# Optimization experiments

Measured on AMD Instinct MI355X. Metric: run time of the kernel, lower is better.

## Reference

```python
import jax, jax.numpy as jnp
import numpy as np

TOP_K = 2  # module default top_k


def setup_inputs() -> dict:
    key = jax.random.key(0)
    k1, k2, k3 = jax.random.split(key, 3)
    B, D, E = 4096, 1024, 64  # tokens, input_dim, num_experts
    return {
        "tensor1": jax.random.normal(k1, (B, D), dtype=jnp.float32),
        "tensor2": jax.random.normal(k2, (B, D), dtype=jnp.float32),
        "gate_weight": jax.random.normal(k3, (E, 2 * D), dtype=jnp.float32) * 0.02,
    }


def reference(tensor1, tensor2, gate_weight):
    # x: (B, 2D)
    x = jnp.concatenate((tensor1, tensor2), axis=-1)
    # pairwise L2 distance between each token and each expert vector
    diff = gate_weight[None, :, :] - x[:, None, :]          # (B, E, 2D)
    logits = -jnp.sqrt(jnp.sum(diff * diff, axis=-1))        # (B, E)
    topk_logits, indices = jax.lax.top_k(logits, TOP_K)      # (B, K)
    gating_weights = jax.nn.softmax(topk_logits, axis=-1)    # (B, K)
    rows = jnp.arange(logits.shape[0])[:, None]              # (B, 1)
    sparse_gating = jnp.zeros_like(logits).at[rows, indices].set(gating_weights)
    return sparse_gating
```

## Files before the change

### kernel.cpp

```cpp
#include <hip/hip_runtime.h>
#include <math.h>

#define NTOK 4096
#define NDIM 1024
#define KTOT 2048
#define NEXP 64
#define MT   64
#define KB   64
#define LSTR 72
#define NKC  16
#define NSTG 2

typedef _Float16 half8 __attribute__((ext_vector_type(8)));
typedef _Float16 half4 __attribute__((ext_vector_type(4)));
typedef float    floatx4 __attribute__((ext_vector_type(4)));

#define XSCALE 16.0f
#define WSCALE 1024.0f
#define INVSCALE (1.0f / (16.0f * 1024.0f))

struct h2pair { _Float16 h, l; };
__device__ __forceinline__ h2pair split2(float v) {
    h2pair r;
    r.h = (_Float16)v;
    r.l = (_Float16)(v - (float)r.h);
    return r;
}

__global__ __launch_bounds__(256, 4) void gemm_mfma(const float* __restrict__ t1,
                                                    const float* __restrict__ t2,
                                                    const float* __restrict__ W,
                                                    float* __restrict__ Gp,
                                                    float* __restrict__ Cp,
                                                    float* __restrict__ Wp) {
    __shared__ _Float16 Xh[MT * LSTR], Xl[MT * LSTR];
    __shared__ _Float16 Wh[NEXP * LSTR], Wl[NEXP * LSTR];

    const int tid  = threadIdx.x;
    const int lane = tid & 63;
    const int wv   = tid >> 6;
    const int srow = tid >> 4;
    const int scol = tid & 15;
    const int kc   = blockIdx.y;
    const int kbase = kc * (NSTG * KB);
    const int tok0  = blockIdx.x * MT;

    const float* __restrict__ xsrc = (kbase < NDIM)
        ? (t1 + (size_t)tok0 * NDIM + kbase)
        : (t2 + (size_t)tok0 * NDIM + (kbase - NDIM));
    const float* __restrict__ wsrc = W + kbase;

    floatx4 acc[4];
    #pragma unroll
    for (int j = 0; j < 4; ++j) { acc[j][0] = 0.f; acc[j][1] = 0.f; acc[j][2] = 0.f; acc[j][3] = 0.f; }
    float ssx[4] = {0.f, 0.f, 0.f, 0.f};
    float ssw[4] = {0.f, 0.f, 0.f, 0.f};

    const int frow = lane & 15;
    const int fq   = lane >> 4;
    const _Float16* xh_p = Xh + (16 * wv + frow) * LSTR + fq * 8;
    const _Float16* xl_p = Xl + (16 * wv + frow) * LSTR + fq * 8;

    #pragma unroll
    for (int s = 0; s < NSTG; ++s) {
        #pragma unroll
        for (int i = 0; i < 4; ++i) {
            const int row = srow + 16 * i;
            const float4 xv = *reinterpret_cast<const float4*>(
                xsrc + (size_t)row * NDIM + s * KB + scol * 4);
            const float4 wq = *reinterpret_cast<const float4*>(
                wsrc + (size_t)row * KTOT + s * KB + scol * 4);
            ssx[i] = fmaf(xv.x, xv.x, fmaf(xv.y, xv.y, fmaf(xv.z, xv.z, fmaf(xv.w, xv.w, ssx[i]))));
            ssw[i] = fmaf(wq.x, wq.x, fmaf(wq.y, wq.y, fmaf(wq.z, wq.z, fmaf(wq.w, wq.w, ssw[i]))));
            const h2pair x0 = split2(xv.x * XSCALE), x1 = split2(xv.y * XSCALE);
            const h2pair x2 = split2(xv.z * XSCALE), x3 = split2(xv.w * XSCALE);
            const h2pair w0 = split2(wq.x * WSCALE), w1 = split2(wq.y * WSCALE);
            const h2pair w2 = split2(wq.z * WSCALE), w3 = split2(wq.w * WSCALE);
            half4 hx, lx, hw, lw;
            hx[0] = x0.h; hx[1] = x1.h; hx[2] = x2.h; hx[3] = x3.h;
            lx[0] = x0.l; lx[1] = x1.l; lx[2] = x2.l; lx[3] = x3.l;
            hw[0] = w0.h; hw[1] = w1.h; hw[2] = w2.h; hw[3] = w3.h;
            lw[0] = w0.l; lw[1] = w1.l; lw[2] = w2.l; lw[3] = w3.l;
            *reinterpret_cast<half4*>(Xh + row * LSTR + scol * 4) = hx;
            *reinterpret_cast<half4*>(Xl + row * LSTR + scol * 4) = lx;
            *reinterpret_cast<half4*>(Wh + row * LSTR + scol * 4) = hw;
            *reinterpret_cast<half4*>(Wl + row * LSTR + scol * 4) = lw;
        }
        __syncthreads();

        #pragma unroll
        for (int ks = 0; ks < 2; ++ks) {
            const int ko = ks * 32;
            const half8 ah = *reinterpret_cast<const half8*>(xh_p + ko);
            const half8 al = *reinterpret_cast<const half8*>(xl_p + ko);
            half8 bh[4], bl[4];
            #pragma unroll
            for (int j = 0; j < 4; ++j) {
                bh[j] = *reinterpret_cast<const half8*>(Wh + (16 * j + frow) * LSTR + fq * 8 + ko);
                bl[j] = *reinterpret_cast<const half8*>(Wl + (16 * j + frow) * LSTR + fq * 8 + ko);
            }
            #pragma unroll
            for (int j = 0; j < 4; ++j)
                acc[j] = __builtin_amdgcn_mfma_f32_16x16x32_f16(ah, bh[j], acc[j], 0, 0, 0);
            #pragma unroll
            for (int j = 0; j < 4; ++j)
                acc[j] = __builtin_amdgcn_mfma_f32_16x16x32_f16(al, bh[j], acc[j], 0, 0, 0);
            #pragma unroll
            for (int j = 0; j < 4; ++j)
                acc[j] = __builtin_amdgcn_mfma_f32_16x16x32_f16(ah, bl[j], acc[j], 0, 0, 0);
        }
        __syncthreads();
    }

    const int m0 = 16 * wv + fq * 4;
    #pragma unroll
    for (int j = 0; j < 4; ++j) {
        #pragma unroll
        for (int i = 0; i < 4; ++i) {
            Gp[((size_t)kc * NTOK + tok0 + m0 + i) * NEXP + 16 * j + frow] = acc[j][i] * INVSCALE;
        }
    }

    #pragma unroll
    for (int off = 1; off < 16; off <<= 1) {
        #pragma unroll
        for (int i = 0; i < 4; ++i) {
            ssx[i] += __shfl_xor(ssx[i], off, 64);
            ssw[i] += __shfl_xor(ssw[i], off, 64);
        }
    }
    if (scol == 0) {
        #pragma unroll
        for (int i = 0; i < 4; ++i)
            Cp[(size_t)kc * NTOK + tok0 + srow + 16 * i] = ssx[i];
        if (blockIdx.x == 0) {
            #pragma unroll
            for (int i = 0; i < 4; ++i)
                Wp[kc * NEXP + srow + 16 * i] = ssw[i];
        }
    }
}

__global__ __launch_bounds__(256) void finalize(const float* __restrict__ Gp,
                                                const float* __restrict__ Cp,
                                                const float* __restrict__ Wp,
                                                float* __restrict__ out) {
    const int wv = threadIdx.x >> 6, lane = threadIdx.x & 63;
    const int token = blockIdx.x * 4 + wv;

    float gsum = 0.f, csum = 0.f, nv = 0.f;
    #pragma unroll
    for (int cix = 0; cix < NKC; ++cix) {
        gsum += Gp[((size_t)cix * NTOK + token) * NEXP + lane];
        csum += Cp[(size_t)cix * NTOK + token];
        nv   += Wp[cix * NEXP + lane];
    }

    const float S = fmaf(-2.f, gsum, csum) + nv;
    const float logit = -sqrtf(S);

    float v1 = logit; int i1 = lane;
    #pragma unroll
    for (int off = 32; off > 0; off >>= 1) {
        float ov = __shfl_xor(v1, off, 64);
        int   oi = __shfl_xor(i1, off, 64);
        if (ov > v1 || (ov == v1 && oi < i1)) { v1 = ov; i1 = oi; }
    }
    float v2 = (lane == i1) ? -__builtin_inff() : logit;
    int   i2 = lane;
    #pragma unroll
    for (int off = 32; off > 0; off >>= 1) {
        float ov = __shfl_xor(v2, off, 64);
        int   oi = __shfl_xor(i2, off, 64);
        if (ov > v2 || (ov == v2 && oi < i2)) { v2 = ov; i2 = oi; }
    }
    const float e2  = expf(v2 - v1);
    const float inv = 1.f / (1.f + e2);
    const float o = (lane == i1) ? inv : ((lane == i2) ? e2 * inv : 0.f);
    out[(size_t)token * NEXP + lane] = o;
}

extern "C" void kernel_launch(void* const* d_in, const int* in_sizes, int n_in,
                              void* d_out, int out_size, void* d_ws, size_t ws_size,
                              hipStream_t stream) {
    const float* t1 = (const float*)d_in[0];
    const float* t2 = (const float*)d_in[1];
    const float* W  = (const float*)d_in[2];
    float* out = (float*)d_out;

    float* Gp = (float*)d_ws;
    float* Cp = Gp + (size_t)NKC * NTOK * NEXP;
    float* Wp = Cp + (size_t)NKC * NTOK;

    gemm_mfma<<<dim3(NTOK / MT, NKC), 256, 0, stream>>>(t1, t2, W, Gp, Cp, Wp);
    finalize<<<NTOK / 4, 256, 0, stream>>>(Gp, Cp, Wp, out);
}
```

Baseline: 89.05 us.

## Precompute split fp16 gate weights once and halve K-split partials

Adds a prep kernel that converts the gate weights into hi/lo fp16 halves and computes the expert norms once, instead of every GEMM block reconverting the fp32 weights. The GEMM then loads the pre-split fp16 weights directly into shared memory. The K-split count drops from 16 to 8 with 4 stages per block, which halves the partial-sum traffic that finalize reads. The cost is an extra kernel launch, fewer blocks in the GEMM grid (512 instead of 1024), and launch bounds relaxed from 4 to 3.

```diff
diff --git a/kernel.cpp b/kernel.cpp
--- a/kernel.cpp
+++ b/kernel.cpp
@@ -8,8 +8,8 @@
 #define MT   64
 #define KB   64
 #define LSTR 72
-#define NKC  16
-#define NSTG 2
+#define NKC  8
+#define NSTG 4
 
 typedef _Float16 half8 __attribute__((ext_vector_type(8)));
 typedef _Float16 half4 __attribute__((ext_vector_type(4)));
@@ -27,12 +27,42 @@
     return r;
 }
 
-__global__ __launch_bounds__(256, 4) void gemm_mfma(const float* __restrict__ t1,
+__global__ __launch_bounds__(256) void prep_w(const float* __restrict__ W,
+                                              _Float16* __restrict__ Whg,
+                                              _Float16* __restrict__ Wlg,
+                                              float* __restrict__ nrm) {
+    const int e = blockIdx.x, t = threadIdx.x;
+    const float* row = W + (size_t)e * KTOT + t * 8;
+    const float4 a = *reinterpret_cast<const float4*>(row);
+    const float4 b = *reinterpret_cast<const float4*>(row + 4);
+    float ss = fmaf(a.x, a.x, fmaf(a.y, a.y, fmaf(a.z, a.z, fmaf(a.w, a.w, 0.f))));
+    ss = fmaf(b.x, b.x, fmaf(b.y, b.y, fmaf(b.z, b.z, fmaf(b.w, b.w, ss))));
+
+    const h2pair p0 = split2(a.x * WSCALE), p1 = split2(a.y * WSCALE);
+    const h2pair p2 = split2(a.z * WSCALE), p3 = split2(a.w * WSCALE);
+    const h2pair p4 = split2(b.x * WSCALE), p5 = split2(b.y * WSCALE);
+    const h2pair p6 = split2(b.z * WSCALE), p7 = split2(b.w * WSCALE);
+    half8 h, l;
+    h[0]=p0.h; h[1]=p1.h; h[2]=p2.h; h[3]=p3.h; h[4]=p4.h; h[5]=p5.h; h[6]=p6.h; h[7]=p7.h;
+    l[0]=p0.l; l[1]=p1.l; l[2]=p2.l; l[3]=p3.l; l[4]=p4.l; l[5]=p5.l; l[6]=p6.l; l[7]=p7.l;
+    *reinterpret_cast<half8*>(Whg + (size_t)e * KTOT + t * 8) = h;
+    *reinterpret_cast<half8*>(Wlg + (size_t)e * KTOT + t * 8) = l;
+
+    #pragma unroll
+    for (int off = 32; off > 0; off >>= 1) ss += __shfl_down(ss, off, 64);
+    __shared__ float red[4];
+    const int lane = t & 63, wv = t >> 6;
+    if (lane == 0) red[wv] = ss;
+    __syncthreads();
+    if (t == 0) nrm[e] = (red[0] + red[1]) + (red[2] + red[3]);
+}
+
+__global__ __launch_bounds__(256, 3) void gemm_mfma(const float* __restrict__ t1,
                                                     const float* __restrict__ t2,
-                                                    const float* __restrict__ W,
+                                                    const _Float16* __restrict__ Whg,
+                                                    const _Float16* __restrict__ Wlg,
                                                     float* __restrict__ Gp,
-                                                    float* __restrict__ Cp,
-                                                    float* __restrict__ Wp) {
+                                                    float* __restrict__ Cp) {
     __shared__ _Float16 Xh[MT * LSTR], Xl[MT * LSTR];
     __shared__ _Float16 Wh[NEXP * LSTR], Wl[NEXP * LSTR];
 
@@ -41,6 +71,8 @@
     const int wv   = tid >> 6;
     const int srow = tid >> 4;
     const int scol = tid & 15;
+    const int wrow = tid >> 2;
+    const int wseg = tid & 3;
     const int kc   = blockIdx.y;
     const int kbase = kc * (NSTG * KB);
     const int tok0  = blockIdx.x * MT;
@@ -48,13 +80,15 @@
     const float* __restrict__ xsrc = (kbase < NDIM)
         ? (t1 + (size_t)tok0 * NDIM + kbase)
         : (t2 + (size_t)tok0 * NDIM + (kbase - NDIM));
-    const float* __restrict__ wsrc = W + kbase;
+    const _Float16* __restrict__ whsrc = Whg + (size_t)wrow * KTOT + kbase + wseg * 16;
+    const _Float16* __restrict__ wlsrc = Wlg + (size_t)wrow * KTOT + kbase + wseg * 16;
+    _Float16* whdst = Wh + wrow * LSTR + wseg * 16;
+    _Float16* wldst = Wl + wrow * LSTR + wseg * 16;
 
     floatx4 acc[4];
     #pragma unroll
     for (int j = 0; j < 4; ++j) { acc[j][0] = 0.f; acc[j][1] = 0.f; acc[j][2] = 0.f; acc[j][3] = 0.f; }
     float ssx[4] = {0.f, 0.f, 0.f, 0.f};
-    float ssw[4] = {0.f, 0.f, 0.f, 0.f};
 
     const int frow = lane & 15;
     const int fq   = lane >> 4;
@@ -63,28 +97,29 @@
 
     #pragma unroll
     for (int s = 0; s < NSTG; ++s) {
+        {
+            const half8 wh0 = *reinterpret_cast<const half8*>(whsrc + s * KB);
+            const half8 wh1 = *reinterpret_cast<const half8*>(whsrc + s * KB + 8);
+            const half8 wl0 = *reinterpret_cast<const half8*>(wlsrc + s * KB);
+            const half8 wl1 = *reinterpret_cast<const half8*>(wlsrc + s * KB + 8);
+            *reinterpret_cast<half8*>(whdst)     = wh0;
+            *reinterpret_cast<half8*>(whdst + 8) = wh1;
+            *reinterpret_cast<half8*>(wldst)     = wl0;
+            *reinterpret_cast<half8*>(wldst + 8) = wl1;
+        }
         #pragma unroll
         for (int i = 0; i < 4; ++i) {
             const int row = srow + 16 * i;
             const float4 xv = *reinterpret_cast<const float4*>(
                 xsrc + (size_t)row * NDIM + s * KB + scol * 4);
-            const float4 wq = *reinterpret_cast<const float4*>(
-                wsrc + (size_t)row * KTOT + s * KB + scol * 4);
             ssx[i] = fmaf(xv.x, xv.x, fmaf(xv.y, xv.y, fmaf(xv.z, xv.z, fmaf(xv.w, xv.w, ssx[i]))));
-            ssw[i] = fmaf(wq.x, wq.x, fmaf(wq.y, wq.y, fmaf(wq.z, wq.z, fmaf(wq.w, wq.w, ssw[i]))));
             const h2pair x0 = split2(xv.x * XSCALE), x1 = split2(xv.y * XSCALE);
             const h2pair x2 = split2(xv.z * XSCALE), x3 = split2(xv.w * XSCALE);
-            const h2pair w0 = split2(wq.x * WSCALE), w1 = split2(wq.y * WSCALE);
-            const h2pair w2 = split2(wq.z * WSCALE), w3 = split2(wq.w * WSCALE);
-            half4 hx, lx, hw, lw;
+            half4 hx, lx;
             hx[0] = x0.h; hx[1] = x1.h; hx[2] = x2.h; hx[3] = x3.h;
             lx[0] = x0.l; lx[1] = x1.l; lx[2] = x2.l; lx[3] = x3.l;
-            hw[0] = w0.h; hw[1] = w1.h; hw[2] = w2.h; hw[3] = w3.h;
-            lw[0] = w0.l; lw[1] = w1.l; lw[2] = w2.l; lw[3] = w3.l;
             *reinterpret_cast<half4*>(Xh + row * LSTR + scol * 4) = hx;
             *reinterpret_cast<half4*>(Xl + row * LSTR + scol * 4) = lx;
-            *reinterpret_cast<half4*>(Wh + row * LSTR + scol * 4) = hw;
-            *reinterpret_cast<half4*>(Wl + row * LSTR + scol * 4) = lw;
         }
         __syncthreads();
 
@@ -117,46 +152,38 @@
     for (int j = 0; j < 4; ++j) {
         #pragma unroll
         for (int i = 0; i < 4; ++i) {
-            Gp[((size_t)kc * NTOK + tok0 + m0 + i) * NEXP + 16 * j + frow] = acc[j][i] * INVSCALE;
+            Gp[((size_t)kc * NTOK + tok0 + m0 + i) * NEXP + 16 * j + frow] = acc[j][i];
         }
     }
 
     #pragma unroll
     for (int off = 1; off < 16; off <<= 1) {
         #pragma unroll
-        for (int i = 0; i < 4; ++i) {
-            ssx[i] += __shfl_xor(ssx[i], off, 64);
-            ssw[i] += __shfl_xor(ssw[i], off, 64);
-        }
+        for (int i = 0; i < 4; ++i) ssx[i] += __shfl_xor(ssx[i], off, 64);
     }
     if (scol == 0) {
         #pragma unroll
         for (int i = 0; i < 4; ++i)
             Cp[(size_t)kc * NTOK + tok0 + srow + 16 * i] = ssx[i];
-        if (blockIdx.x == 0) {
-            #pragma unroll
-            for (int i = 0; i < 4; ++i)
-                Wp[kc * NEXP + srow + 16 * i] = ssw[i];
-        }
     }
 }
 
 __global__ __launch_bounds__(256) void finalize(const float* __restrict__ Gp,
                                                 const float* __restrict__ Cp,
-                                                const float* __restrict__ Wp,
+                                                const float* __restrict__ nrm,
                                                 float* __restrict__ out) {
     const int wv = threadIdx.x >> 6, lane = threadIdx.x & 63;
     const int token = blockIdx.x * 4 + wv;
 
-    float gsum = 0.f, csum = 0.f, nv = 0.f;
+    float gsum = 0.f, csum = 0.f;
     #pragma unroll
     for (int cix = 0; cix < NKC; ++cix) {
         gsum += Gp[((size_t)cix * NTOK + token) * NEXP + lane];
         csum += Cp[(size_t)cix * NTOK + token];
-        nv   += Wp[cix * NEXP + lane];
-    }
-
-    const float S = fmaf(-2.f, gsum, csum) + nv;
+    }
+    const float nv = nrm[lane];
+
+    const float S = fmaf(-2.f * INVSCALE, gsum, csum) + nv;
     const float logit = -sqrtf(S);
 
     float v1 = logit; int i1 = lane;
@@ -188,10 +215,14 @@
     const float* W  = (const float*)d_in[2];
     float* out = (float*)d_out;
 
-    float* Gp = (float*)d_ws;
-    float* Cp = Gp + (size_t)NKC * NTOK * NEXP;
-    float* Wp = Cp + (size_t)NKC * NTOK;
-
-    gemm_mfma<<<dim3(NTOK / MT, NKC), 256, 0, stream>>>(t1, t2, W, Gp, Cp, Wp);
-    finalize<<<NTOK / 4, 256, 0, stream>>>(Gp, Cp, Wp, out);
-}
+    char* ws = (char*)d_ws;
+    float*    Gp  = (float*)ws;
+    float*    Cp  = Gp + (size_t)NKC * NTOK * NEXP;
+    float*    nrm = Cp + (size_t)NKC * NTOK;
+    _Float16* Whg = (_Float16*)(nrm + NEXP);
+    _Float16* Wlg = Whg + (size_t)NEXP * KTOT;
+
+    prep_w<<<NEXP, 256, 0, stream>>>(W, Whg, Wlg, nrm);
+    gemm_mfma<<<dim3(NTOK / MT, NKC), 256, 0, stream>>>(t1, t2, Whg, Wlg, Gp, Cp);
+    finalize<<<NTOK / 4, 256, 0, stream>>>(Gp, Cp, nrm, out);
+}
```

New measurement: 88.98 us. Within noise of the previous version (-0.1%).
